# Optimization experiments

Measured on AMD Instinct MI355X. Metric: run time of the kernel, lower is better.

## Reference

```python
import jax, jax.numpy as jnp
import numpy as np

PROJ_DIM = 768
NUM_HEADS = 12
HEAD_DIM = PROJ_DIM // NUM_HEADS  # 64
GRID_H, GRID_W = 32, 32
SEQ = GRID_H * GRID_W  # 1024
BATCH = 8
HALF = HEAD_DIM // 2      # 32
QUARTER = HALF // 2       # 16


def _rope_tables():
    freq = 1.0 / (10000.0 ** (jnp.arange(QUARTER, dtype=jnp.float32) / QUARTER))
    rows = jnp.repeat(jnp.arange(GRID_H, dtype=jnp.float32), GRID_W)   # (SEQ,)
    cols = jnp.tile(jnp.arange(GRID_W, dtype=jnp.float32), GRID_H)     # (SEQ,)
    ar = rows[:, None] * freq[None, :]  # (SEQ, QUARTER)
    ac = cols[:, None] * freq[None, :]
    return jnp.cos(ar), jnp.sin(ar), jnp.cos(ac), jnp.sin(ac)


def _rotate(x, cos, sin):
    # x: (B, H, S, 2*QUARTER); cos/sin: (S, QUARTER) broadcast over B,H
    x_even = x[..., 0::2]
    x_odd = x[..., 1::2]
    r_even = x_even * cos - x_odd * sin
    r_odd = x_even * sin + x_odd * cos
    return jnp.stack([r_even, r_odd], axis=-1).reshape(x.shape)


def _apply_rope_2d(x, cr, sr, cc, sc):
    x_row = _rotate(x[..., :HALF], cr, sr)
    x_col = _rotate(x[..., HALF:], cc, sc)
    return jnp.concatenate([x_row, x_col], axis=-1)


def setup_inputs() -> dict:
    key = jax.random.key(0)
    ks = jax.random.split(key, 9)
    d = PROJ_DIM
    s = 1.0 / np.sqrt(d)
    return {
        "x": jax.random.normal(ks[0], (BATCH, SEQ, d), dtype=jnp.float32),
        "Wq": jax.random.normal(ks[1], (d, d), dtype=jnp.float32) * s,
        "bq": jnp.zeros((d,), dtype=jnp.float32),
        "Wk": jax.random.normal(ks[2], (d, d), dtype=jnp.float32) * s,
        "bk": jnp.zeros((d,), dtype=jnp.float32),
        "Wv": jax.random.normal(ks[3], (d, d), dtype=jnp.float32) * s,
        "bv": jnp.zeros((d,), dtype=jnp.float32),
        "Wo": jax.random.normal(ks[4], (d, d), dtype=jnp.float32) * s,
        "bo": jnp.zeros((d,), dtype=jnp.float32),
    }


def reference(x, Wq, bq, Wk, bk, Wv, bv, Wo, bo):
    B, S, D = x.shape
    cr, sr, cc, sc = _rope_tables()

    def split_heads(t):
        return t.reshape(B, S, NUM_HEADS, HEAD_DIM).transpose(0, 2, 1, 3)

    q = split_heads(x @ Wq + bq)
    k = split_heads(x @ Wk + bk)
    v = split_heads(x @ Wv + bv)

    q = _apply_rope_2d(q, cr, sr, cc, sc)
    k = _apply_rope_2d(k, cr, sr, cc, sc)

    scale = jnp.float32(np.sqrt(HEAD_DIM))
    attn = jnp.einsum('bhqd,bhkd->bhqk', q, k) / scale
    attn = jax.nn.softmax(attn, axis=-1)
    out = jnp.einsum('bhqk,bhkd->bhqd', attn, v)
    out = out.transpose(0, 2, 1, 3).reshape(B, S, D)
    return out @ Wo + bo
```

## Files before the change

### kernel.cpp

```cpp
#include <hip/hip_runtime.h>
#include <hip/hip_bf16.h>
#include <math.h>

typedef __attribute__((ext_vector_type(8))) short short8;
typedef __attribute__((ext_vector_type(8))) _Float16 half8;
typedef __attribute__((ext_vector_type(4))) float floatx4;
typedef const unsigned int __attribute__((address_space(1))) as1_cu32;
typedef unsigned int __attribute__((address_space(3))) as3_u32;

__device__ __forceinline__ unsigned short h16(float x) {
  union { _Float16 f; unsigned short u; } c; c.f = (_Float16)x; return c.u;
}
__device__ __forceinline__ float h2f(unsigned short u) {
  union { _Float16 f; unsigned short u; } c; c.u = u; return (float)c.f;
}
__device__ __forceinline__ void hsplit(float x, unsigned short& h, unsigned short& l) {
  h = h16(x); l = h16(x - h2f(h));
}

__global__ void rope_tab_kernel(float* __restrict__ tab) {
  int idx = blockIdx.x * 256 + threadIdx.x;
  if (idx >= 32768) return;
  int s  = idx >> 5, k2 = idx & 31;
  int r  = s >> 5,  c  = s & 31;
  int j  = k2 & 15;
  float f   = expf(-(float)j * (9.210340371976184f / 16.0f));
  float pos = (k2 < 16) ? (float)r : (float)c;
  float a   = pos * f;
  tab[2*idx]   = cosf(a);
  tab[2*idx+1] = sinf(a);
}

__global__ __launch_bounds__(256) void xconv_kernel(
    const float* __restrict__ x, unsigned short* __restrict__ xh,
    unsigned short* __restrict__ xl) {
  int i = (blockIdx.x * 256 + threadIdx.x) * 4;
  float4 f = *(const float4*)&x[i];
  ushort4 h, l;
  hsplit(f.x, h.x, l.x); hsplit(f.y, h.y, l.y);
  hsplit(f.z, h.z, l.z); hsplit(f.w, h.w, l.w);
  *(ushort4*)&xh[i] = h;
  *(ushort4*)&xl[i] = l;
}

__global__ __launch_bounds__(256) void wconv_kernel(
    const float* __restrict__ Wq, const float* __restrict__ Wk,
    const float* __restrict__ Wv, const float* __restrict__ Wo,
    unsigned short* __restrict__ wt, unsigned short* __restrict__ wo) {
  __shared__ float tile[32][33];
  int z = blockIdx.z;
  const float* src = (z == 0) ? Wq : (z == 1) ? Wk : (z == 2) ? Wv : Wo;
  unsigned short* dh = (z < 3) ? wt + (size_t)z * 589824 : wo;
  int k0 = blockIdx.x * 32, n0 = blockIdx.y * 32;
  int tx = threadIdx.x & 31, ty = threadIdx.x >> 5;
#pragma unroll
  for (int r = 0; r < 4; ++r)
    tile[ty + r * 8][tx] = src[(size_t)(k0 + ty + r * 8) * 768 + n0 + tx];
  __syncthreads();
#pragma unroll
  for (int r = 0; r < 4; ++r) {
    int n = n0 + ty + r * 8;
    dh[(size_t)n * 768 + k0 + tx] = h16(tile[tx][ty + r * 8]);
  }
}

__device__ __forceinline__ void stage_tile(const unsigned short* __restrict__ src,
                                           int row0, int k0, short* lds, int t) {
  int l  = t & 63;
  int wb = t & 192;
#pragma unroll
  for (int r = 0; r < 2; ++r) {
    int cbase = r * 256 + wb;
    int c = cbase + l;
    int m = c >> 2, s = c & 3;
    int g = s ^ (m & 3);
    const unsigned short* gp = src + (size_t)(row0 + m) * 768 + k0 + g * 8;
    __builtin_amdgcn_global_load_lds((as1_cu32*)(const void*)gp,
                                     (as3_u32*)(void*)(lds + cbase * 8),
                                     16, 0, 0);
  }
}

#define GEMM_MAIN_LOOP_DB(Ah, Al, Bs, m0, n0)                                    \
  floatx4 acc[4][4];                                                             \
  _Pragma("unroll") for (int i = 0; i < 4; ++i)                                  \
      _Pragma("unroll") for (int j = 0; j < 4; ++j)                              \
          acc[i][j] = (floatx4){0.f, 0.f, 0.f, 0.f};                             \
  const int l  = t & 63;                                                         \
  const int lm = l & 15, g = l >> 4;                                             \
  const int wm = ((t >> 7) & 1) * 64, wn = ((t >> 6) & 1) * 64;                  \
  const int sl = g ^ (lm & 3);                                                   \
  stage_tile(Ah, m0, 0, sAh, t);                                                 \
  stage_tile(Al, m0, 0, sAl, t);                                                 \
  stage_tile(Bs, n0, 0, sB, t);                                                  \
  for (int k0 = 0; k0 < 768; k0 += 32) {                                         \
    __syncthreads();                                                             \
    const int cur = (k0 >> 5) & 1, nxt = cur ^ 1;                                \
    if (k0 + 32 < 768) {                                                         \
      stage_tile(Ah, m0, k0 + 32, sAh + nxt * 4096, t);                          \
      stage_tile(Al, m0, k0 + 32, sAl + nxt * 4096, t);                          \
      stage_tile(Bs, n0, k0 + 32, sB  + nxt * 4096, t);                          \
    }                                                                            \
    const short* cAh = sAh + cur * 4096;                                         \
    const short* cAl = sAl + cur * 4096;                                         \
    const short* cB  = sB  + cur * 4096;                                         \
    half8 ah[4], al[4];                                                          \
    _Pragma("unroll") for (int i = 0; i < 4; ++i) {                              \
      int ra = wm + i * 16 + lm;                                                 \
      ah[i] = *(const half8*)&cAh[ra * 32 + sl * 8];                             \
      al[i] = *(const half8*)&cAl[ra * 32 + sl * 8];                             \
    }                                                                            \
    _Pragma("unroll") for (int j = 0; j < 4; ++j) {                              \
      int rb = wn + j * 16 + lm;                                                 \
      half8 b8 = *(const half8*)&cB[rb * 32 + sl * 8];                           \
      _Pragma("unroll") for (int i = 0; i < 4; ++i) {                            \
        acc[i][j] = __builtin_amdgcn_mfma_f32_16x16x32_f16(ah[i], b8, acc[i][j], 0, 0, 0); \
        acc[i][j] = __builtin_amdgcn_mfma_f32_16x16x32_f16(al[i], b8, acc[i][j], 0, 0, 0); \
      }                                                                          \
    }                                                                            \
  }

__global__ __launch_bounds__(256) void qk_mfma_kernel(
    const unsigned short* __restrict__ xh, const unsigned short* __restrict__ xl,
    const unsigned short* __restrict__ wt,
    const float* __restrict__ bq, const float* __restrict__ bk,
    const float* __restrict__ tab,
    unsigned short* __restrict__ qhp, unsigned short* __restrict__ qlp,
    unsigned short* __restrict__ khp) {
  __shared__ __align__(16) short sAh[8192], sAl[8192], sB[8192];
  const int t  = threadIdx.x;
  const int m0 = blockIdx.x * 128;
  const int n0 = blockIdx.y * 128;

  GEMM_MAIN_LOOP_DB(xh, xl, wt, m0, n0)

  const int proj = n0 / 768;
  const int col0 = n0 % 768;
  const float* bias = (proj == 0) ? bq : bk;
  const float qs = (proj == 0) ? 0.125f : 1.f;

#pragma unroll
  for (int j = 0; j < 4; ++j) {
    int colf = col0 + wn + j * 16;
    int hh = colf >> 6;
    int d  = (colf & 63) + lm;
    float bsv = bias[colf + lm];
    int kidx = (d < 32) ? (d >> 1) : (16 + ((d - 32) >> 1));
    float sgn = (d & 1) ? 1.f : -1.f;
#pragma unroll
    for (int i = 0; i < 4; ++i) {
#pragma unroll
      for (int r = 0; r < 4; ++r) {
        int m = m0 + wm + i * 16 + g * 4 + r;
        int b = m >> 10, sidx = m & 1023;
        float val = acc[i][j][r] + bsv;
        float2 cssn = *(const float2*)&tab[(sidx * 32 + kidx) * 2];
        float p = __shfl_xor(val, 1);
        val = (val * cssn.x + sgn * (p * cssn.y)) * qs;
        size_t off = (((size_t)(b * 12 + hh)) * 1024 + sidx) * 64 + (d & ~1);
        if (proj == 0) {
          unsigned short hv, lv; hsplit(val, hv, lv);
          unsigned hx = (unsigned)__shfl_xor((int)hv, 1);
          unsigned lx = (unsigned)__shfl_xor((int)lv, 1);
          if ((lm & 1) == 0)
            *(unsigned*)&qhp[off] = ((hx & 0xffffu) << 16) | (unsigned)hv;
          else
            *(unsigned*)&qlp[off] = (((unsigned)lv) << 16) | (lx & 0xffffu);
        } else {
          unsigned short hv = h16(val);
          unsigned hx = (unsigned)__shfl_xor((int)hv, 1);
          if ((lm & 1) == 0)
            *(unsigned*)&khp[off] = ((hx & 0xffffu) << 16) | (unsigned)hv;
        }
      }
    }
  }
}

__global__ __launch_bounds__(256) void v_mfma_kernel(
    const unsigned short* __restrict__ xh, const unsigned short* __restrict__ xl,
    const unsigned short* __restrict__ wv_, const float* __restrict__ bv,
    unsigned short* __restrict__ vtp) {
  __shared__ __align__(16) short smem[24576];
  short* sAh = smem;          short* sAl = smem + 8192;
  short* sB  = smem + 16384;
  const int t  = threadIdx.x;
  const int m0 = blockIdx.x * 128;
  const int n0 = blockIdx.y * 128;

  GEMM_MAIN_LOOP_DB(xh, xl, wv_, m0, n0)

  uint2 hpk[4][4];
#pragma unroll
  for (int j = 0; j < 4; ++j) {
    float bsv = bv[n0 + wn + j * 16 + lm];
#pragma unroll
    for (int i = 0; i < 4; ++i) {
      unsigned short hv[4];
#pragma unroll
      for (int r = 0; r < 4; ++r) hv[r] = h16(acc[i][j][r] + bsv);
      hpk[i][j] = make_uint2((unsigned)hv[0] | ((unsigned)hv[1] << 16),
                             (unsigned)hv[2] | ((unsigned)hv[3] << 16));
    }
  }
  const int bidx = m0 >> 10;
  const int s0   = m0 & 1023;

  __syncthreads();
#pragma unroll
  for (int i = 0; i < 4; ++i)
#pragma unroll
    for (int j = 0; j < 4; ++j) {
      int n  = wn + j * 16 + lm;
      int mb = wm + i * 16 + g * 4;
      int chunk = mb >> 3;
      int cs = chunk ^ (n & 7);
      *(uint2*)&smem[n * 128 + cs * 8 + (g & 1) * 4] = hpk[i][j];
    }
  __syncthreads();
  {
    int nl = t >> 1, hf = t & 1;
    int colf = n0 + nl;
    int hh = colf >> 6, d = colf & 63;
    size_t rb = ((size_t)(bidx * 12 + hh) * 64 + d) * 1024 + s0;
#pragma unroll
    for (int cc = 0; cc < 8; ++cc) {
      int c = hf * 8 + cc;
      int cs = c ^ (nl & 7);
      *(short8*)&vtp[rb + c * 8] = *(const short8*)&smem[nl * 128 + cs * 8];
    }
  }
}

__global__ __launch_bounds__(256) void attn_mfma_kernel(
    const unsigned short* __restrict__ qhp, const unsigned short* __restrict__ qlp,
    const unsigned short* __restrict__ khp, const unsigned short* __restrict__ vtp,
    unsigned short* __restrict__ oh, unsigned short* __restrict__ ol) {
  __shared__ __align__(16) short sK[8192], sVT[8192];
  __shared__ __align__(16) short sP[4][2304];
  const int t  = threadIdx.x;
  const int wv = t >> 6, l = t & 63, lm = l & 15, g = l >> 4;
  const int bh  = blockIdx.x >> 3;
  const int qw0 = (blockIdx.x & 7) * 128 + wv * 32;

  half8 qfh[2][2], qfl[2][2];
#pragma unroll
  for (int i = 0; i < 2; ++i) {
    size_t base = ((size_t)bh * 1024 + qw0 + i * 16 + lm) * 64;
#pragma unroll
    for (int tt = 0; tt < 2; ++tt) {
      qfh[i][tt] = *(const half8*)&qhp[base + tt * 32 + g * 8];
      qfl[i][tt] = *(const half8*)&qlp[base + tt * 32 + g * 8];
    }
  }

  float mrun[2] = {-1e30f, -1e30f}, lrun[2] = {0.f, 0.f};
  floatx4 o[2][4];
#pragma unroll
  for (int i = 0; i < 2; ++i)
#pragma unroll
    for (int jd = 0; jd < 4; ++jd) o[i][jd] = (floatx4){0.f, 0.f, 0.f, 0.f};

  short* sPw = sP[wv];

  auto stage_kv = [&](int kt, int buf) {
#pragma unroll
    for (int qi = 0; qi < 4; ++qi) {
      int cz = qi * 256 + t;
      int plane = cz >> 9;
      int c = cz & 511;
      int row = c >> 3, s = c & 7;
      int gs = s ^ (row & 7);
      const unsigned short* gp = plane
          ? vtp + ((size_t)bh * 64 + row) * 1024 + kt * 64 + gs * 8
          : khp + ((size_t)bh * 1024 + kt * 64 + row) * 64 + gs * 8;
      short* dst = (plane ? sVT : sK) + buf * 4096 + c * 8;
      __builtin_amdgcn_global_load_lds((as1_cu32*)(const void*)gp,
                                       (as3_u32*)(void*)dst, 16, 0, 0);
    }
  };

  stage_kv(0, 0);

#pragma unroll 1
  for (int kt = 0; kt < 16; ++kt) {
    __syncthreads();
    const int cur = kt & 1, nxt = cur ^ 1;
    if (kt + 1 < 16) stage_kv(kt + 1, nxt);
    const short* cK  = sK  + cur * 4096;
    const short* cVT = sVT + cur * 4096;

    floatx4 sacc[2][4];
#pragma unroll
    for (int i = 0; i < 2; ++i)
#pragma unroll
      for (int j = 0; j < 4; ++j) sacc[i][j] = (floatx4){0.f, 0.f, 0.f, 0.f};
#pragma unroll
    for (int tt = 0; tt < 2; ++tt) {
#pragma unroll
      for (int j = 0; j < 4; ++j) {
        int row = j * 16 + lm;
        int so = ((4 * tt + g) ^ (row & 7)) * 8;
        half8 kf = *(const half8*)&cK[row * 64 + so];
#pragma unroll
        for (int i = 0; i < 2; ++i) {
          sacc[i][j] = __builtin_amdgcn_mfma_f32_16x16x32_f16(kf, qfh[i][tt], sacc[i][j], 0, 0, 0);
          sacc[i][j] = __builtin_amdgcn_mfma_f32_16x16x32_f16(kf, qfl[i][tt], sacc[i][j], 0, 0, 0);
        }
      }
    }

    float p[2][16];
#pragma unroll
    for (int i = 0; i < 2; ++i) {
      float mt = -1e30f;
#pragma unroll
      for (int j = 0; j < 4; ++j)
#pragma unroll
        for (int r = 0; r < 4; ++r) mt = fmaxf(mt, sacc[i][j][r]);
      mt = fmaxf(mt, __shfl_xor(mt, 16));
      mt = fmaxf(mt, __shfl_xor(mt, 32));
      float mn = fmaxf(mrun[i], mt);
      float corr = __expf(mrun[i] - mn);
      mrun[i] = mn;
      float ps = 0.f;
#pragma unroll
      for (int j = 0; j < 4; ++j)
#pragma unroll
        for (int r = 0; r < 4; ++r) {
          float e = __expf(sacc[i][j][r] - mn);
          p[i][j * 4 + r] = e; ps += e;
        }
      ps += __shfl_xor(ps, 16);
      ps += __shfl_xor(ps, 32);
      lrun[i] = lrun[i] * corr + ps;
#pragma unroll
      for (int jd = 0; jd < 4; ++jd)
#pragma unroll
        for (int r = 0; r < 4; ++r) o[i][jd][r] *= corr;
    }

#pragma unroll
    for (int i = 0; i < 2; ++i)
#pragma unroll
      for (int j = 0; j < 4; ++j) {
        unsigned short hv[4];
#pragma unroll
        for (int r = 0; r < 4; ++r) hv[r] = h16(p[i][j * 4 + r]);
        *(uint2*)&sPw[(i * 16 + lm) * 72 + j * 16 + g * 4] =
            make_uint2((unsigned)hv[0] | ((unsigned)hv[1] << 16),
                       (unsigned)hv[2] | ((unsigned)hv[3] << 16));
      }
    half8 pf[2][2];
#pragma unroll
    for (int i = 0; i < 2; ++i)
#pragma unroll
      for (int tt = 0; tt < 2; ++tt)
        pf[i][tt] = *(const half8*)&sPw[(i * 16 + lm) * 72 + tt * 32 + g * 8];

#pragma unroll
    for (int tt = 0; tt < 2; ++tt) {
#pragma unroll
      for (int jd = 0; jd < 4; ++jd) {
        int row = jd * 16 + lm;
        int so = ((4 * tt + g) ^ (row & 7)) * 8;
        half8 vf = *(const half8*)&cVT[row * 64 + so];
#pragma unroll
        for (int i = 0; i < 2; ++i)
          o[i][jd] = __builtin_amdgcn_mfma_f32_16x16x32_f16(vf, pf[i][tt], o[i][jd], 0, 0, 0);
      }
    }
  }

  const int b = bh / 12, h = bh % 12;
#pragma unroll
  for (int i = 0; i < 2; ++i) {
    float inv = 1.f / lrun[i];
    int q = qw0 + i * 16 + lm;
#pragma unroll
    for (int jd = 0; jd < 4; ++jd) {
      unsigned short hv[4], lv[4];
#pragma unroll
      for (int r = 0; r < 4; ++r) hsplit(o[i][jd][r] * inv, hv[r], lv[r]);
      size_t off = ((size_t)(b * 1024) + q) * 768 + h * 64 + jd * 16 + g * 4;
      *(uint2*)&oh[off] = make_uint2((unsigned)hv[0] | ((unsigned)hv[1] << 16),
                                     (unsigned)hv[2] | ((unsigned)hv[3] << 16));
      *(uint2*)&ol[off] = make_uint2((unsigned)lv[0] | ((unsigned)lv[1] << 16),
                                     (unsigned)lv[2] | ((unsigned)lv[3] << 16));
    }
  }
}

__global__ __launch_bounds__(256) void proj_mfma_kernel(
    const unsigned short* __restrict__ ah_, const unsigned short* __restrict__ al_,
    const unsigned short* __restrict__ wo_, const float* __restrict__ bo,
    float* __restrict__ out) {
  __shared__ __align__(16) short sAh[8192], sAl[8192], sB[8192];
  const int t  = threadIdx.x;
  const int m0 = blockIdx.x * 128;
  const int n0 = blockIdx.y * 128;

  GEMM_MAIN_LOOP_DB(ah_, al_, wo_, m0, n0)

#pragma unroll
  for (int j = 0; j < 4; ++j) {
    int n = n0 + wn + j * 16 + lm;
    float bsv = bo[n];
#pragma unroll
    for (int i = 0; i < 4; ++i) {
#pragma unroll
      for (int r = 0; r < 4; ++r) {
        int m = m0 + wm + i * 16 + g * 4 + r;
        out[(size_t)m * 768 + n] = acc[i][j][r] + bsv;
      }
    }
  }
}

extern "C" void kernel_launch(void* const* d_in, const int* in_sizes, int n_in,
                              void* d_out, int out_size, void* d_ws, size_t ws_size,
                              hipStream_t stream) {
  const float* x  = (const float*)d_in[0];
  const float* Wq = (const float*)d_in[1];
  const float* bq = (const float*)d_in[2];
  const float* Wk = (const float*)d_in[3];
  const float* bk = (const float*)d_in[4];
  const float* Wv = (const float*)d_in[5];
  const float* bv = (const float*)d_in[6];
  const float* Wo = (const float*)d_in[7];
  const float* bo = (const float*)d_in[8];
  float* out = (float*)d_out;

  char* w = (char*)d_ws;
  float* tab          = (float*)(w);
  unsigned short* wt  = (unsigned short*)(w + 262144);
  unsigned short* wo  = (unsigned short*)(w + 3801088);
  unsigned short* xh  = (unsigned short*)(w + 4980736);
  unsigned short* xl  = (unsigned short*)(w + 17563648);
  unsigned short* qh  = (unsigned short*)(w + 30146560);
  unsigned short* ql  = (unsigned short*)(w + 42729472);
  unsigned short* kh  = (unsigned short*)(w + 55312384);
  unsigned short* vt  = (unsigned short*)(w + 67895296);

  rope_tab_kernel<<<dim3(128), dim3(256), 0, stream>>>(tab);
  xconv_kernel<<<dim3(6144), dim3(256), 0, stream>>>(x, xh, xl);
  wconv_kernel<<<dim3(24, 24, 4), dim3(256), 0, stream>>>(
      Wq, Wk, Wv, Wo, wt, wo);
  qk_mfma_kernel<<<dim3(64, 12), dim3(256), 0, stream>>>(
      xh, xl, wt, bq, bk, tab, qh, ql, kh);
  v_mfma_kernel<<<dim3(64, 6), dim3(256), 0, stream>>>(
      xh, xl, wt + (size_t)2 * 589824, bv, vt);
  attn_mfma_kernel<<<dim3(768), dim3(256), 0, stream>>>(
      qh, ql, kh, vt, xh, xl);
  proj_mfma_kernel<<<dim3(64, 6), dim3(256), 0, stream>>>(
      xh, xl, wo, bo, out);
}
```

Baseline: 271.9 us.

## Fuse QKV GEMMs, add lazy softmax rescale, priorities, and smaller proj tiles

Merges the Q/K and V projection kernels into one launch with an 18-wide column grid, so a single kernel fills the GPU instead of two back-to-back launches. In attention it remaps block indices, raises wave priority around the MFMA sections, and skips the running-max update and output rescale when the new tile max stays within 8 of the running max. The output projection moves to 64-row tiles with twice as many blocks for better occupancy. The lazy rescale lets exponents grow up to e^8 before correction, which raises overflow risk in the fp16 P values.

New measurement: 279.1 us. 1.03x slower.

```diff
diff --git a/kernel.cpp b/kernel.cpp
--- a/kernel.cpp
+++ b/kernel.cpp
@@ -79,6 +79,16 @@
                                      (as3_u32*)(void*)(lds + cbase * 8),
                                      16, 0, 0);
   }
+}
+__device__ __forceinline__ void stage_tile64(const unsigned short* __restrict__ src,
+                                             int row0, int k0, short* lds, int t) {
+  int c = t;
+  int m = c >> 2, s = c & 3;
+  int g = s ^ (m & 3);
+  const unsigned short* gp = src + (size_t)(row0 + m) * 768 + k0 + g * 8;
+  __builtin_amdgcn_global_load_lds((as1_cu32*)(const void*)gp,
+                                   (as3_u32*)(void*)(lds + c * 8),
+                                   16, 0, 0);
 }
 
 #define GEMM_MAIN_LOOP_DB(Ah, Al, Bs, m0, n0)                                    \
@@ -120,67 +130,13 @@
     }                                                                            \
   }
 
-__global__ __launch_bounds__(256) void qk_mfma_kernel(
+__global__ __launch_bounds__(256) void qkv_mfma_kernel(
     const unsigned short* __restrict__ xh, const unsigned short* __restrict__ xl,
     const unsigned short* __restrict__ wt,
     const float* __restrict__ bq, const float* __restrict__ bk,
-    const float* __restrict__ tab,
+    const float* __restrict__ bv, const float* __restrict__ tab,
     unsigned short* __restrict__ qhp, unsigned short* __restrict__ qlp,
-    unsigned short* __restrict__ khp) {
-  __shared__ __align__(16) short sAh[8192], sAl[8192], sB[8192];
-  const int t  = threadIdx.x;
-  const int m0 = blockIdx.x * 128;
-  const int n0 = blockIdx.y * 128;
-
-  GEMM_MAIN_LOOP_DB(xh, xl, wt, m0, n0)
-
-  const int proj = n0 / 768;
-  const int col0 = n0 % 768;
-  const float* bias = (proj == 0) ? bq : bk;
-  const float qs = (proj == 0) ? 0.125f : 1.f;
-
-#pragma unroll
-  for (int j = 0; j < 4; ++j) {
-    int colf = col0 + wn + j * 16;
-    int hh = colf >> 6;
-    int d  = (colf & 63) + lm;
-    float bsv = bias[colf + lm];
-    int kidx = (d < 32) ? (d >> 1) : (16 + ((d - 32) >> 1));
-    float sgn = (d & 1) ? 1.f : -1.f;
-#pragma unroll
-    for (int i = 0; i < 4; ++i) {
-#pragma unroll
-      for (int r = 0; r < 4; ++r) {
-        int m = m0 + wm + i * 16 + g * 4 + r;
-        int b = m >> 10, sidx = m & 1023;
-        float val = acc[i][j][r] + bsv;
-        float2 cssn = *(const float2*)&tab[(sidx * 32 + kidx) * 2];
-        float p = __shfl_xor(val, 1);
-        val = (val * cssn.x + sgn * (p * cssn.y)) * qs;
-        size_t off = (((size_t)(b * 12 + hh)) * 1024 + sidx) * 64 + (d & ~1);
-        if (proj == 0) {
-          unsigned short hv, lv; hsplit(val, hv, lv);
-          unsigned hx = (unsigned)__shfl_xor((int)hv, 1);
-          unsigned lx = (unsigned)__shfl_xor((int)lv, 1);
-          if ((lm & 1) == 0)
-            *(unsigned*)&qhp[off] = ((hx & 0xffffu) << 16) | (unsigned)hv;
-          else
-            *(unsigned*)&qlp[off] = (((unsigned)lv) << 16) | (lx & 0xffffu);
-        } else {
-          unsigned short hv = h16(val);
-          unsigned hx = (unsigned)__shfl_xor((int)hv, 1);
-          if ((lm & 1) == 0)
-            *(unsigned*)&khp[off] = ((hx & 0xffffu) << 16) | (unsigned)hv;
-        }
-      }
-    }
-  }
-}
-
-__global__ __launch_bounds__(256) void v_mfma_kernel(
-    const unsigned short* __restrict__ xh, const unsigned short* __restrict__ xl,
-    const unsigned short* __restrict__ wv_, const float* __restrict__ bv,
-    unsigned short* __restrict__ vtp) {
+    unsigned short* __restrict__ khp, unsigned short* __restrict__ vtp) {
   __shared__ __align__(16) short smem[24576];
   short* sAh = smem;          short* sAl = smem + 8192;
   short* sB  = smem + 16384;
@@ -188,46 +144,89 @@
   const int m0 = blockIdx.x * 128;
   const int n0 = blockIdx.y * 128;
 
-  GEMM_MAIN_LOOP_DB(xh, xl, wv_, m0, n0)
-
-  uint2 hpk[4][4];
-#pragma unroll
-  for (int j = 0; j < 4; ++j) {
-    float bsv = bv[n0 + wn + j * 16 + lm];
-#pragma unroll
-    for (int i = 0; i < 4; ++i) {
-      unsigned short hv[4];
-#pragma unroll
-      for (int r = 0; r < 4; ++r) hv[r] = h16(acc[i][j][r] + bsv);
-      hpk[i][j] = make_uint2((unsigned)hv[0] | ((unsigned)hv[1] << 16),
-                             (unsigned)hv[2] | ((unsigned)hv[3] << 16));
-    }
-  }
-  const int bidx = m0 >> 10;
-  const int s0   = m0 & 1023;
-
-  __syncthreads();
-#pragma unroll
-  for (int i = 0; i < 4; ++i)
+  GEMM_MAIN_LOOP_DB(xh, xl, wt, m0, n0)
+
+  const int proj = n0 / 768;
+  const int col0 = n0 % 768;
+
+  if (proj < 2) {
+    const float* bias = (proj == 0) ? bq : bk;
+    const float qs = (proj == 0) ? 0.125f : 1.f;
 #pragma unroll
     for (int j = 0; j < 4; ++j) {
-      int n  = wn + j * 16 + lm;
-      int mb = wm + i * 16 + g * 4;
-      int chunk = mb >> 3;
-      int cs = chunk ^ (n & 7);
-      *(uint2*)&smem[n * 128 + cs * 8 + (g & 1) * 4] = hpk[i][j];
-    }
-  __syncthreads();
-  {
-    int nl = t >> 1, hf = t & 1;
-    int colf = n0 + nl;
-    int hh = colf >> 6, d = colf & 63;
-    size_t rb = ((size_t)(bidx * 12 + hh) * 64 + d) * 1024 + s0;
-#pragma unroll
-    for (int cc = 0; cc < 8; ++cc) {
-      int c = hf * 8 + cc;
-      int cs = c ^ (nl & 7);
-      *(short8*)&vtp[rb + c * 8] = *(const short8*)&smem[nl * 128 + cs * 8];
+      int colf = col0 + wn + j * 16;
+      int hh = colf >> 6;
+      int d  = (colf & 63) + lm;
+      float bsv = bias[colf + lm];
+      int kidx = (d < 32) ? (d >> 1) : (16 + ((d - 32) >> 1));
+      float sgn = (d & 1) ? 1.f : -1.f;
+#pragma unroll
+      for (int i = 0; i < 4; ++i) {
+#pragma unroll
+        for (int r = 0; r < 4; ++r) {
+          int m = m0 + wm + i * 16 + g * 4 + r;
+          int b = m >> 10, sidx = m & 1023;
+          float val = acc[i][j][r] + bsv;
+          float2 cssn = *(const float2*)&tab[(sidx * 32 + kidx) * 2];
+          float p = __shfl_xor(val, 1);
+          val = (val * cssn.x + sgn * (p * cssn.y)) * qs;
+          size_t off = (((size_t)(b * 12 + hh)) * 1024 + sidx) * 64 + (d & ~1);
+          if (proj == 0) {
+            unsigned short hv, lv; hsplit(val, hv, lv);
+            unsigned hx = (unsigned)__shfl_xor((int)hv, 1);
+            unsigned lx = (unsigned)__shfl_xor((int)lv, 1);
+            if ((lm & 1) == 0)
+              *(unsigned*)&qhp[off] = ((hx & 0xffffu) << 16) | (unsigned)hv;
+            else
+              *(unsigned*)&qlp[off] = (((unsigned)lv) << 16) | (lx & 0xffffu);
+          } else {
+            unsigned short hv = h16(val);
+            unsigned hx = (unsigned)__shfl_xor((int)hv, 1);
+            if ((lm & 1) == 0)
+              *(unsigned*)&khp[off] = ((hx & 0xffffu) << 16) | (unsigned)hv;
+          }
+        }
+      }
+    }
+  } else {
+    uint2 hpk[4][4];
+#pragma unroll
+    for (int j = 0; j < 4; ++j) {
+      float bsv = bv[col0 + wn + j * 16 + lm];
+#pragma unroll
+      for (int i = 0; i < 4; ++i) {
+        unsigned short hv[4];
+#pragma unroll
+        for (int r = 0; r < 4; ++r) hv[r] = h16(acc[i][j][r] + bsv);
+        hpk[i][j] = make_uint2((unsigned)hv[0] | ((unsigned)hv[1] << 16),
+                               (unsigned)hv[2] | ((unsigned)hv[3] << 16));
+      }
+    }
+    const int bidx = m0 >> 10;
+    const int s0   = m0 & 1023;
+    __syncthreads();
+#pragma unroll
+    for (int i = 0; i < 4; ++i)
+#pragma unroll
+      for (int j = 0; j < 4; ++j) {
+        int n  = wn + j * 16 + lm;
+        int mb = wm + i * 16 + g * 4;
+        int chunk = mb >> 3;
+        int cs = chunk ^ (n & 7);
+        *(uint2*)&smem[n * 128 + cs * 8 + (g & 1) * 4] = hpk[i][j];
+      }
+    __syncthreads();
+    {
+      int nl = t >> 1, hf = t & 1;
+      int colf = col0 + nl;
+      int hh = colf >> 6, d = colf & 63;
+      size_t rb = ((size_t)(bidx * 12 + hh) * 64 + d) * 1024 + s0;
+#pragma unroll
+      for (int cc = 0; cc < 8; ++cc) {
+        int c = hf * 8 + cc;
+        int cs = c ^ (nl & 7);
+        *(short8*)&vtp[rb + c * 8] = *(const short8*)&smem[nl * 128 + cs * 8];
+      }
     }
   }
 }
@@ -240,8 +239,9 @@
   __shared__ __align__(16) short sP[4][2304];
   const int t  = threadIdx.x;
   const int wv = t >> 6, l = t & 63, lm = l & 15, g = l >> 4;
-  const int bh  = blockIdx.x >> 3;
-  const int qw0 = (blockIdx.x & 7) * 128 + wv * 32;
+  const int bid = blockIdx.x;
+  const int bh  = (bid & 7) + ((bid >> 6) << 3);
+  const int qw0 = ((bid >> 3) & 7) * 128 + wv * 32;
 
   half8 qfh[2][2], qfl[2][2];
 #pragma unroll
@@ -295,6 +295,7 @@
     for (int i = 0; i < 2; ++i)
 #pragma unroll
       for (int j = 0; j < 4; ++j) sacc[i][j] = (floatx4){0.f, 0.f, 0.f, 0.f};
+    __builtin_amdgcn_s_setprio(1);
 #pragma unroll
     for (int tt = 0; tt < 2; ++tt) {
 #pragma unroll
@@ -309,20 +310,27 @@
         }
       }
     }
-
+    __builtin_amdgcn_s_setprio(0);
+
+    float mt[2];
+#pragma unroll
+    for (int i = 0; i < 2; ++i) {
+      float m_ = -1e30f;
+#pragma unroll
+      for (int j = 0; j < 4; ++j)
+#pragma unroll
+        for (int r = 0; r < 4; ++r) m_ = fmaxf(m_, sacc[i][j][r]);
+      m_ = fmaxf(m_, __shfl_xor(m_, 16));
+      m_ = fmaxf(m_, __shfl_xor(m_, 32));
+      mt[i] = m_;
+    }
+    const bool skip = __all((mt[0] <= mrun[0] + 8.f) & (mt[1] <= mrun[1] + 8.f));
     float p[2][16];
 #pragma unroll
     for (int i = 0; i < 2; ++i) {
-      float mt = -1e30f;
-#pragma unroll
-      for (int j = 0; j < 4; ++j)
-#pragma unroll
-        for (int r = 0; r < 4; ++r) mt = fmaxf(mt, sacc[i][j][r]);
-      mt = fmaxf(mt, __shfl_xor(mt, 16));
-      mt = fmaxf(mt, __shfl_xor(mt, 32));
-      float mn = fmaxf(mrun[i], mt);
-      float corr = __expf(mrun[i] - mn);
-      mrun[i] = mn;
+      float mn, corr;
+      if (skip) { mn = mrun[i]; corr = 1.f; }
+      else { mn = fmaxf(mrun[i], mt[i]); corr = __expf(mrun[i] - mn); mrun[i] = mn; }
       float ps = 0.f;
 #pragma unroll
       for (int j = 0; j < 4; ++j)
@@ -334,10 +342,12 @@
       ps += __shfl_xor(ps, 16);
       ps += __shfl_xor(ps, 32);
       lrun[i] = lrun[i] * corr + ps;
-#pragma unroll
-      for (int jd = 0; jd < 4; ++jd)
-#pragma unroll
-        for (int r = 0; r < 4; ++r) o[i][jd][r] *= corr;
+      if (!skip) {
+#pragma unroll
+        for (int jd = 0; jd < 4; ++jd)
+#pragma unroll
+          for (int r = 0; r < 4; ++r) o[i][jd][r] *= corr;
+      }
     }
 
 #pragma unroll
@@ -358,6 +368,7 @@
       for (int tt = 0; tt < 2; ++tt)
         pf[i][tt] = *(const half8*)&sPw[(i * 16 + lm) * 72 + tt * 32 + g * 8];
 
+    __builtin_amdgcn_s_setprio(1);
 #pragma unroll
     for (int tt = 0; tt < 2; ++tt) {
 #pragma unroll
@@ -370,6 +381,7 @@
           o[i][jd] = __builtin_amdgcn_mfma_f32_16x16x32_f16(vf, pf[i][tt], o[i][jd], 0, 0, 0);
       }
     }
+    __builtin_amdgcn_s_setprio(0);
   }
 
   const int b = bh / 12, h = bh % 12;
@@ -395,19 +407,61 @@
     const unsigned short* __restrict__ ah_, const unsigned short* __restrict__ al_,
     const unsigned short* __restrict__ wo_, const float* __restrict__ bo,
     float* __restrict__ out) {
-  __shared__ __align__(16) short sAh[8192], sAl[8192], sB[8192];
+  __shared__ __align__(16) short sAh[4096], sAl[4096], sB[8192];
   const int t  = threadIdx.x;
-  const int m0 = blockIdx.x * 128;
+  const int m0 = blockIdx.x * 64;
   const int n0 = blockIdx.y * 128;
 
-  GEMM_MAIN_LOOP_DB(ah_, al_, wo_, m0, n0)
+  floatx4 acc[2][4];
+#pragma unroll
+  for (int i = 0; i < 2; ++i)
+#pragma unroll
+    for (int j = 0; j < 4; ++j) acc[i][j] = (floatx4){0.f, 0.f, 0.f, 0.f};
+  const int l  = t & 63;
+  const int lm = l & 15, g = l >> 4;
+  const int wm = ((t >> 7) & 1) * 32, wn = ((t >> 6) & 1) * 64;
+  const int sl = g ^ (lm & 3);
+
+  stage_tile64(ah_, m0, 0, sAh, t);
+  stage_tile64(al_, m0, 0, sAl, t);
+  stage_tile (wo_, n0, 0, sB,  t);
+
+  for (int k0 = 0; k0 < 768; k0 += 32) {
+    __syncthreads();
+    const int cur = (k0 >> 5) & 1, nxt = cur ^ 1;
+    if (k0 + 32 < 768) {
+      stage_tile64(ah_, m0, k0 + 32, sAh + nxt * 2048, t);
+      stage_tile64(al_, m0, k0 + 32, sAl + nxt * 2048, t);
+      stage_tile (wo_, n0, k0 + 32, sB  + nxt * 4096, t);
+    }
+    const short* cAh = sAh + cur * 2048;
+    const short* cAl = sAl + cur * 2048;
+    const short* cB  = sB  + cur * 4096;
+    half8 ah[2], al[2];
+#pragma unroll
+    for (int i = 0; i < 2; ++i) {
+      int ra = wm + i * 16 + lm;
+      ah[i] = *(const half8*)&cAh[ra * 32 + sl * 8];
+      al[i] = *(const half8*)&cAl[ra * 32 + sl * 8];
+    }
+#pragma unroll
+    for (int j = 0; j < 4; ++j) {
+      int rb = wn + j * 16 + lm;
+      half8 b8 = *(const half8*)&cB[rb * 32 + sl * 8];
+#pragma unroll
+      for (int i = 0; i < 2; ++i) {
+        acc[i][j] = __builtin_amdgcn_mfma_f32_16x16x32_f16(ah[i], b8, acc[i][j], 0, 0, 0);
+        acc[i][j] = __builtin_amdgcn_mfma_f32_16x16x32_f16(al[i], b8, acc[i][j], 0, 0, 0);
+      }
+    }
+  }
 
 #pragma unroll
   for (int j = 0; j < 4; ++j) {
     int n = n0 + wn + j * 16 + lm;
     float bsv = bo[n];
 #pragma unroll
-    for (int i = 0; i < 4; ++i) {
+    for (int i = 0; i < 2; ++i) {
 #pragma unroll
       for (int r = 0; r < 4; ++r) {
         int m = m0 + wm + i * 16 + g * 4 + r;
@@ -446,12 +500,10 @@
   xconv_kernel<<<dim3(6144), dim3(256), 0, stream>>>(x, xh, xl);
   wconv_kernel<<<dim3(24, 24, 4), dim3(256), 0, stream>>>(
       Wq, Wk, Wv, Wo, wt, wo);
-  qk_mfma_kernel<<<dim3(64, 12), dim3(256), 0, stream>>>(
-      xh, xl, wt, bq, bk, tab, qh, ql, kh);
-  v_mfma_kernel<<<dim3(64, 6), dim3(256), 0, stream>>>(
-      xh, xl, wt + (size_t)2 * 589824, bv, vt);
+  qkv_mfma_kernel<<<dim3(64, 18), dim3(256), 0, stream>>>(
+      xh, xl, wt, bq, bk, bv, tab, qh, ql, kh, vt);
   attn_mfma_kernel<<<dim3(768), dim3(256), 0, stream>>>(
       qh, ql, kh, vt, xh, xl);
-  proj_mfma_kernel<<<dim3(64, 6), dim3(256), 0, stream>>>(
+  proj_mfma_kernel<<<dim3(128, 6), dim3(256), 0, stream>>>(
       xh, xl, wo, bo, out);
 }
```
